# Performance work log

Hardware: AMD Instinct MI355X
Metric: run time of the kernel (lower is better)

The kernel has to match this reference:

```python
import jax, jax.numpy as jnp
import numpy as np

B, T, D = 4, 2048, 1024
H = 16
HD = D // H

def setup_inputs() -> dict:
    key = jax.random.key(0)
    ks = jax.random.split(key, 3)
    x = jax.random.normal(ks[0], (B, T, D), dtype=jnp.float32)
    w_qkv = jax.random.normal(ks[1], (D, 3 * D), dtype=jnp.float32) * (1.0 / np.sqrt(D))
    b_qkv = jnp.zeros((3 * D,), dtype=jnp.float32)
    w_proj = jax.random.normal(ks[2], (D, D), dtype=jnp.float32) * (1.0 / np.sqrt(D))
    b_proj = jnp.zeros((D,), dtype=jnp.float32)
    return {"x": x, "w_qkv": w_qkv, "b_qkv": b_qkv, "w_proj": w_proj, "b_proj": b_proj}

def reference(x, w_qkv, b_qkv, w_proj, b_proj):
    b, t, c = x.shape
    qkv = x @ w_qkv + b_qkv                      # [B,T,3D]
    qkv = qkv.reshape(b, t, 3, H, HD).transpose(2, 0, 3, 1, 4)  # [3,B,H,T,HD]
    q, k, v = qkv[0], qkv[1], qkv[2]
    scale = jnp.sqrt(jnp.asarray(HD, dtype=x.dtype))
    attn = jnp.einsum('bhqd,bhkd->bhqk', q, k) / scale  # [B,H,T,T]
    causal = jnp.tril(jnp.ones((t, t), dtype=bool))
    attn = jnp.where(causal[None, None], attn, -jnp.inf)
    attn = jax.nn.softmax(attn, axis=-1)
    out = jnp.einsum('bhqk,bhkd->bhqd', attn, v)        # [B,H,T,HD]
    out = out.transpose(0, 2, 1, 3).reshape(b, t, c)
    return out @ w_proj + b_proj
```

## Files before the change

### kernel.cpp

```cpp
#include <hip/hip_runtime.h>

typedef float f32x4 __attribute__((ext_vector_type(4)));
typedef __bf16 bf16x8 __attribute__((ext_vector_type(8)));

static __device__ __forceinline__ unsigned short f2bf(float f) {
    unsigned int u = __builtin_bit_cast(unsigned int, f);
    u += 0x7fffu + ((u >> 16) & 1u);
    return (unsigned short)(u >> 16);
}
static __device__ __forceinline__ unsigned short bfc(float f) {
    return __builtin_bit_cast(unsigned short, (__bf16)f);
}

#define QSC 0.18033688011112042f

typedef const __attribute__((address_space(1))) unsigned int gu32;
typedef __attribute__((address_space(3))) unsigned int lu32;
static __device__ __forceinline__ void gload_lds16(const unsigned short* g, unsigned short* l) {
    __builtin_amdgcn_global_load_lds((gu32*)g, (lu32*)l, 16, 0, 0);
}

__global__ __launch_bounds__(256)
void cvt_bf16(const float* __restrict__ in, unsigned short* __restrict__ out) {
    int i = blockIdx.x * 256 + threadIdx.x;
    const float4* p = (const float4*)in + (size_t)i * 2;
    float4 a = p[0], b = p[1];
    union { unsigned short s[8]; uint4 v; } u;
    u.s[0] = f2bf(a.x); u.s[1] = f2bf(a.y); u.s[2] = f2bf(a.z); u.s[3] = f2bf(a.w);
    u.s[4] = f2bf(b.x); u.s[5] = f2bf(b.y); u.s[6] = f2bf(b.z); u.s[7] = f2bf(b.w);
    ((uint4*)out)[i] = u.v;
}

__global__ __launch_bounds__(256)
void transpose_w(const float* __restrict__ w, unsigned short* __restrict__ wT,
                 int K, int N) {
    __shared__ unsigned short Lt[64][65];
    const int k0 = blockIdx.x * 64, n0 = blockIdx.y * 64;
    const int t = threadIdx.x;
    const int r = t >> 4, c4 = (t & 15) * 4;
    #pragma unroll
    for (int i = 0; i < 4; i++) {
        int rr = r + i * 16;
        float4 v = *(const float4*)(w + (k0 + rr) * N + n0 + c4);
        Lt[rr][c4 + 0] = f2bf(v.x); Lt[rr][c4 + 1] = f2bf(v.y);
        Lt[rr][c4 + 2] = f2bf(v.z); Lt[rr][c4 + 3] = f2bf(v.w);
    }
    __syncthreads();
    const int rn = t >> 3, ks = (t & 7) * 8;
    #pragma unroll
    for (int i = 0; i < 2; i++) {
        int rr = rn + i * 32;
        unsigned short tmp[8];
        #pragma unroll
        for (int j = 0; j < 8; j++) tmp[j] = Lt[ks + j][rr];
        *(uint4*)(wT + (n0 + rr) * K + k0 + ks) = *(const uint4*)tmp;
    }
}

__global__ __launch_bounds__(256)
void qkv_gemm2(const unsigned short* __restrict__ A,
               const unsigned short* __restrict__ Bt,
               const float* __restrict__ bias,
               unsigned short* __restrict__ q_ws,
               unsigned short* __restrict__ k_ws,
               unsigned short* __restrict__ vT_ws)
{
    const int K = 1024;
    __shared__ unsigned short LD[16384];
    const int tid = threadIdx.x;
    const int lane = tid & 63, w = tid >> 6;
    const int l15 = lane & 15, lhi = lane >> 4;
    const int m0 = blockIdx.x * 128, n0 = blockIdx.y * 128;
    const int wm = (w >> 1) * 64, wn = (w & 1) * 64;

    const int srow = w * 32 + (lane >> 2);
    const int sg = ((lane & 3) ^ ((lane >> 3) & 3)) * 8;
    const unsigned short* ga = A + (size_t)(m0 + srow) * K + sg;
    const unsigned short* gb = Bt + (size_t)(n0 + srow) * K + sg;
    const int lofs = w * 32 * 32;

    const int rc = (lhi ^ ((l15 >> 1) & 3)) * 8;

    #define ALp(c) (LD + (c) * 4096)
    #define BLp(c) (LD + 8192 + (c) * 4096)

    f32x4 acc[4][4] = {};

    gload_lds16(ga, ALp(0) + lofs);
    gload_lds16(ga + 16 * K, ALp(0) + lofs + 512);
    gload_lds16(gb, BLp(0) + lofs);
    gload_lds16(gb + 16 * K, BLp(0) + lofs + 512);
    __syncthreads();

    int cur = 0;
    for (int k0 = 0; k0 < K; k0 += 32) {
        const int nxt = cur ^ 1;
        if (k0 + 32 < K) {
            gload_lds16(ga + k0 + 32,          ALp(nxt) + lofs);
            gload_lds16(ga + k0 + 32 + 16 * K, ALp(nxt) + lofs + 512);
            gload_lds16(gb + k0 + 32,          BLp(nxt) + lofs);
            gload_lds16(gb + k0 + 32 + 16 * K, BLp(nxt) + lofs + 512);
        }
        bf16x8 af[4], bfr[4];
        #pragma unroll
        for (int m = 0; m < 4; m++)
            af[m] = *(const bf16x8*)(ALp(cur) + (wm + m * 16 + l15) * 32 + rc);
        #pragma unroll
        for (int n = 0; n < 4; n++)
            bfr[n] = *(const bf16x8*)(BLp(cur) + (wn + n * 16 + l15) * 32 + rc);
        __builtin_amdgcn_s_setprio(1);
        #pragma unroll
        for (int m = 0; m < 4; m++)
            #pragma unroll
            for (int n = 0; n < 4; n++)
                acc[m][n] = __builtin_amdgcn_mfma_f32_16x16x32_bf16(af[m], bfr[n], acc[m][n], 0, 0, 0);
        __builtin_amdgcn_s_setprio(0);
        __syncthreads();
        cur = nxt;
    }

    const int which = n0 >> 10;
    if (which == 2) {
        #pragma unroll
        for (int n = 0; n < 4; n++) {
            int col = n0 + wn + n * 16 + l15;
            float bv = bias[col];
            int d = col & 1023;
            int h = d >> 6, hd = d & 63;
            #pragma unroll
            for (int m = 0; m < 4; m++) {
                int row0 = m0 + wm + m * 16 + lhi * 4;
                int b = row0 >> 11, t0 = row0 & 2047;
                ushort4 pk;
                pk.x = f2bf(acc[m][n][0] + bv);
                pk.y = f2bf(acc[m][n][1] + bv);
                pk.z = f2bf(acc[m][n][2] + bv);
                pk.w = f2bf(acc[m][n][3] + bv);
                *(ushort4*)(&vT_ws[((size_t)(b * 16 + h) * 64 + hd) * 2048 + t0]) = pk;
            }
        }
    } else {
        const float qs = (which == 0) ? QSC : 1.0f;
        unsigned short* q_or_k = (which == 0) ? q_ws : k_ws;
        __syncthreads();
        #pragma unroll
        for (int n = 0; n < 4; n++) {
            int col = wn + n * 16 + l15;
            float bv = bias[n0 + col];
            #pragma unroll
            for (int m = 0; m < 4; m++) {
                #pragma unroll
                for (int j = 0; j < 4; j++) {
                    int r = wm + m * 16 + lhi * 4 + j;
                    LD[r * 128 + col] = f2bf((acc[m][n][j] + bv) * qs);
                }
            }
        }
        __syncthreads();
        const int cbase = n0 & 1023;
        #pragma unroll
        for (int i = 0; i < 8; i++) {
            int e = i * 256 + tid;
            int r = e >> 4, c = (e & 15) * 8;
            uint4 v = *(const uint4*)(&LD[r * 128 + c]);
            int grow = m0 + r;
            int b = grow >> 11, t = grow & 2047;
            int gc = cbase + c;
            int h = gc >> 6, hd = gc & 63;
            *(uint4*)(&q_or_k[((size_t)(b * 16 + h) * 2048 + t) * 64 + hd]) = v;
        }
    }
    #undef ALp
    #undef BLp
}

#define LKK 72

__global__ __launch_bounds__(256, 2)
void attn_fwd(const unsigned short* __restrict__ q_ws,
              const unsigned short* __restrict__ k_ws,
              const unsigned short* __restrict__ vT_ws,
              unsigned short* __restrict__ attn_ws)
{
    __shared__ unsigned short Kb[2][64 * LKK];
    __shared__ unsigned short Vb[2][64 * LKK];
    __shared__ unsigned short Pl[4][2][16 * 64];

    const int bh = blockIdx.x;
    const int qb = 15 - blockIdx.y;
    const int b = bh >> 4, h = bh & 15;
    const int tid = threadIdx.x;
    const int lane = tid & 63, wid = tid >> 6;
    const int l15 = lane & 15, lhi = lane >> 4;
    const int tbase = bh * 2048;
    const float NINF = -__builtin_inff();

    const int r0 = tid >> 2;
    const int c0 = (tid & 3) * 16;
    const unsigned short* kg = k_ws + (size_t)(tbase + r0) * 64 + c0;
    const unsigned short* vg = vT_ws + ((size_t)bh * 64 + r0) * 2048 + c0;

    const int xr = l15 & 7;

    bf16x8 ones;
    #pragma unroll
    for (int z = 0; z < 8; z++) ones[z] = (__bf16)1.0f;

    const int qrow = qb * 128 + wid * 32;
    const int nkv = 2 * (qb + 1);

    bf16x8 qf[2][2];
    #pragma unroll
    for (int m = 0; m < 2; m++)
        #pragma unroll
        for (int ks = 0; ks < 2; ks++)
            qf[m][ks] = *(const bf16x8*)(q_ws + (size_t)(tbase + qrow + m * 16 + l15) * 64 + ks * 32 + lhi * 8);

    f32x4 o[2][4] = {};
    f32x4 osum[2] = {};

    *(uint4*)(&Kb[0][r0 * LKK + c0])     = *(const uint4*)(kg);
    *(uint4*)(&Kb[0][r0 * LKK + c0 + 8]) = *(const uint4*)(kg + 8);
    *(uint4*)(&Vb[0][r0 * LKK + c0])     = *(const uint4*)(vg);
    *(uint4*)(&Vb[0][r0 * LKK + c0 + 8]) = *(const uint4*)(vg + 8);
    __syncthreads();

    int cur = 0;
    for (int kb = 0; kb < nkv; ++kb) {
        const int k0 = kb * 64;
        const int knx = (kb + 1 < nkv ? kb + 1 : kb) * 64;
        uint4 ka0 = *(const uint4*)(kg + (size_t)knx * 64);
        uint4 ka1 = *(const uint4*)(kg + (size_t)knx * 64 + 8);
        uint4 va0 = *(const uint4*)(vg + knx);
        uint4 va1 = *(const uint4*)(vg + knx + 8);

        if (k0 <= qrow + 31) {
            f32x4 s[2][4] = {};
            __builtin_amdgcn_s_setprio(1);
            #pragma unroll
            for (int ks = 0; ks < 2; ks++) {
                bf16x8 kf[4];
                #pragma unroll
                for (int n = 0; n < 4; n++)
                    kf[n] = *(const bf16x8*)(&Kb[cur][(n * 16 + l15) * LKK + ks * 32 + lhi * 8]);
                #pragma unroll
                for (int m = 0; m < 2; m++)
                    #pragma unroll
                    for (int n = 0; n < 4; n++)
                        s[m][n] = __builtin_amdgcn_mfma_f32_16x16x32_bf16(kf[n], qf[m][ks], s[m][n], 0, 0, 0);
            }
            __builtin_amdgcn_s_setprio(0);
            if (k0 + 63 > qrow) {
                #pragma unroll
                for (int m = 0; m < 2; m++) {
                    int qg = qrow + m * 16 + l15;
                    #pragma unroll
                    for (int n = 0; n < 4; n++) {
                        int kgl = k0 + n * 16 + lhi * 4;
                        #pragma unroll
                        for (int j = 0; j < 4; j++)
                            s[m][n][j] = (kgl + j <= qg) ? s[m][n][j] : NINF;
                    }
                }
            }
            #pragma unroll
            for (int m = 0; m < 2; m++)
                #pragma unroll
                for (int n = 0; n < 4; n++)
                    #pragma unroll
                    for (int j = 0; j < 4; j++)
                        s[m][n][j] = exp2f(s[m][n][j]);
            #pragma unroll
            for (int m = 0; m < 2; m++)
                #pragma unroll
                for (int n = 0; n < 4; n++) {
                    ushort4 pk;
                    pk.x = bfc(s[m][n][0]); pk.y = bfc(s[m][n][1]);
                    pk.z = bfc(s[m][n][2]); pk.w = bfc(s[m][n][3]);
                    int chunk = (2 * n + (lhi >> 1)) ^ xr;
                    *(ushort4*)(&Pl[wid][m][l15 * 64 + chunk * 8 + (lhi & 1) * 4]) = pk;
                }
            __builtin_amdgcn_s_setprio(1);
            #pragma unroll
            for (int ks = 0; ks < 2; ks++) {
                int chunk = (4 * ks + lhi) ^ xr;
                bf16x8 vf[4];
                #pragma unroll
                for (int nd = 0; nd < 4; nd++)
                    vf[nd] = *(const bf16x8*)(&Vb[cur][(nd * 16 + l15) * LKK + ks * 32 + lhi * 8]);
                #pragma unroll
                for (int m = 0; m < 2; m++) {
                    bf16x8 pf = *(const bf16x8*)(&Pl[wid][m][l15 * 64 + chunk * 8]);
                    #pragma unroll
                    for (int nd = 0; nd < 4; nd++)
                        o[m][nd] = __builtin_amdgcn_mfma_f32_16x16x32_bf16(pf, vf[nd], o[m][nd], 0, 0, 0);
                    osum[m] = __builtin_amdgcn_mfma_f32_16x16x32_bf16(pf, ones, osum[m], 0, 0, 0);
                }
            }
            __builtin_amdgcn_s_setprio(0);
        }
        *(uint4*)(&Kb[cur ^ 1][r0 * LKK + c0])     = ka0;
        *(uint4*)(&Kb[cur ^ 1][r0 * LKK + c0 + 8]) = ka1;
        *(uint4*)(&Vb[cur ^ 1][r0 * LKK + c0])     = va0;
        *(uint4*)(&Vb[cur ^ 1][r0 * LKK + c0 + 8]) = va1;
        __syncthreads();
        cur ^= 1;
    }
    #pragma unroll
    for (int m = 0; m < 2; m++) {
        #pragma unroll
        for (int j = 0; j < 4; j++) {
            float inv = 1.0f / osum[m][j];
            int t = qrow + m * 16 + lhi * 4 + j;
            #pragma unroll
            for (int nd = 0; nd < 4; nd++) {
                int d = nd * 16 + l15;
                attn_ws[((size_t)(b * 2048 + t) * 16 + h) * 64 + d] = f2bf(o[m][nd][j] * inv);
            }
        }
    }
}

__global__ __launch_bounds__(256)
void proj_gemm2(const unsigned short* __restrict__ A,
                const unsigned short* __restrict__ Bt,
                const float* __restrict__ bias, float* __restrict__ out)
{
    const int K = 1024, N = 1024;
    __shared__ unsigned short Al[2][128 * 32];
    __shared__ unsigned short Bl[2][128 * 32];
    const int tid = threadIdx.x;
    const int lane = tid & 63, w = tid >> 6;
    const int l15 = lane & 15, lhi = lane >> 4;
    const int m0 = blockIdx.x * 128, n0 = blockIdx.y * 128;
    const int wm = (w >> 1) * 64, wn = (w & 1) * 64;

    const int srow = w * 32 + (lane >> 2);
    const int sg = ((lane & 3) ^ ((lane >> 3) & 3)) * 8;
    const unsigned short* ga = A + (size_t)(m0 + srow) * K + sg;
    const unsigned short* gb = Bt + (size_t)(n0 + srow) * K + sg;
    const int lofs = w * 32 * 32;

    const int rc = (lhi ^ ((l15 >> 1) & 3)) * 8;

    f32x4 acc[4][4] = {};

    gload_lds16(ga, &Al[0][lofs]);
    gload_lds16(ga + 16 * K, &Al[0][lofs + 512]);
    gload_lds16(gb, &Bl[0][lofs]);
    gload_lds16(gb + 16 * K, &Bl[0][lofs + 512]);
    __syncthreads();

    int cur = 0;
    for (int k0 = 0; k0 < K; k0 += 32) {
        const int nxt = cur ^ 1;
        if (k0 + 32 < K) {
            gload_lds16(ga + k0 + 32,          &Al[nxt][lofs]);
            gload_lds16(ga + k0 + 32 + 16 * K, &Al[nxt][lofs + 512]);
            gload_lds16(gb + k0 + 32,          &Bl[nxt][lofs]);
            gload_lds16(gb + k0 + 32 + 16 * K, &Bl[nxt][lofs + 512]);
        }
        bf16x8 af[4], bfr[4];
        #pragma unroll
        for (int m = 0; m < 4; m++)
            af[m] = *(const bf16x8*)(&Al[cur][(wm + m * 16 + l15) * 32 + rc]);
        #pragma unroll
        for (int n = 0; n < 4; n++)
            bfr[n] = *(const bf16x8*)(&Bl[cur][(wn + n * 16 + l15) * 32 + rc]);
        __builtin_amdgcn_s_setprio(1);
        #pragma unroll
        for (int m = 0; m < 4; m++)
            #pragma unroll
            for (int n = 0; n < 4; n++)
                acc[m][n] = __builtin_amdgcn_mfma_f32_16x16x32_bf16(af[m], bfr[n], acc[m][n], 0, 0, 0);
        __builtin_amdgcn_s_setprio(0);
        __syncthreads();
        cur = nxt;
    }

    #pragma unroll
    for (int n = 0; n < 4; n++) {
        int col = n0 + wn + n * 16 + l15;
        float bv = bias[col];
        #pragma unroll
        for (int m = 0; m < 4; m++)
            #pragma unroll
            for (int j = 0; j < 4; j++) {
                int row = m0 + wm + m * 16 + lhi * 4 + j;
                out[row * N + col] = acc[m][n][j] + bv;
            }
    }
}

extern "C" void kernel_launch(void* const* d_in, const int* in_sizes, int n_in,
                              void* d_out, int out_size, void* d_ws, size_t ws_size,
                              hipStream_t stream)
{
    const float* x      = (const float*)d_in[0];
    const float* w_qkv  = (const float*)d_in[1];
    const float* b_qkv  = (const float*)d_in[2];
    const float* w_proj = (const float*)d_in[3];
    const float* b_proj = (const float*)d_in[4];
    float* out = (float*)d_out;

    const size_t SEG = (size_t)8 * 1024 * 1024;
    unsigned short* q_ws    = (unsigned short*)d_ws;
    unsigned short* k_ws    = q_ws + SEG;
    unsigned short* vT_ws   = k_ws + SEG;
    unsigned short* attn_ws = vT_ws + SEG;

    unsigned short* x_bf   = (unsigned short*)d_out;
    unsigned short* wqkvT  = x_bf + SEG;
    unsigned short* wprojT = q_ws;

    cvt_bf16<<<4096, 256, 0, stream>>>(x, x_bf);
    transpose_w<<<dim3(16, 48), 256, 0, stream>>>(w_qkv, wqkvT, 1024, 3072);
    qkv_gemm2<<<dim3(64, 24), 256, 0, stream>>>(x_bf, wqkvT, b_qkv, q_ws, k_ws, vT_ws);
    attn_fwd<<<dim3(64, 16), 256, 0, stream>>>(q_ws, k_ws, vT_ws, attn_ws);
    transpose_w<<<dim3(16, 16), 256, 0, stream>>>(w_proj, wprojT, 1024, 1024);
    proj_gemm2<<<dim3(64, 8), 256, 0, stream>>>(attn_ws, wprojT, b_proj, out);
}
```

Baseline: 165.4 us.

## Fuse fp32-to-bf16 conversion of x into QKV GEMM A-tile loading

Result: slower. 173.0 us (+4.6%).

```diff
diff --git a/kernel.cpp b/kernel.cpp
--- a/kernel.cpp
+++ b/kernel.cpp
@@ -18,17 +18,6 @@
 typedef __attribute__((address_space(3))) unsigned int lu32;
 static __device__ __forceinline__ void gload_lds16(const unsigned short* g, unsigned short* l) {
     __builtin_amdgcn_global_load_lds((gu32*)g, (lu32*)l, 16, 0, 0);
-}
-
-__global__ __launch_bounds__(256)
-void cvt_bf16(const float* __restrict__ in, unsigned short* __restrict__ out) {
-    int i = blockIdx.x * 256 + threadIdx.x;
-    const float4* p = (const float4*)in + (size_t)i * 2;
-    float4 a = p[0], b = p[1];
-    union { unsigned short s[8]; uint4 v; } u;
-    u.s[0] = f2bf(a.x); u.s[1] = f2bf(a.y); u.s[2] = f2bf(a.z); u.s[3] = f2bf(a.w);
-    u.s[4] = f2bf(b.x); u.s[5] = f2bf(b.y); u.s[6] = f2bf(b.z); u.s[7] = f2bf(b.w);
-    ((uint4*)out)[i] = u.v;
 }
 
 __global__ __launch_bounds__(256)
@@ -58,7 +47,7 @@
 }
 
 __global__ __launch_bounds__(256)
-void qkv_gemm2(const unsigned short* __restrict__ A,
+void qkv_gemm2(const float* __restrict__ X,
                const unsigned short* __restrict__ Bt,
                const float* __restrict__ bias,
                unsigned short* __restrict__ q_ws,
@@ -75,8 +64,8 @@
 
     const int srow = w * 32 + (lane >> 2);
     const int sg = ((lane & 3) ^ ((lane >> 3) & 3)) * 8;
-    const unsigned short* ga = A + (size_t)(m0 + srow) * K + sg;
-    const unsigned short* gb = Bt + (size_t)(n0 + srow) * K + sg;
+    const float*          gaf = X  + (size_t)(m0 + srow) * K + sg;
+    const unsigned short* gb  = Bt + (size_t)(n0 + srow) * K + sg;
     const int lofs = w * 32 * 32;
 
     const int rc = (lhi ^ ((l15 >> 1) & 3)) * 8;
@@ -86,18 +75,33 @@
 
     f32x4 acc[4][4] = {};
 
-    gload_lds16(ga, ALp(0) + lofs);
-    gload_lds16(ga + 16 * K, ALp(0) + lofs + 512);
-    gload_lds16(gb, BLp(0) + lofs);
-    gload_lds16(gb + 16 * K, BLp(0) + lofs + 512);
+    {
+        float4 a0 = *(const float4*)(gaf);
+        float4 a1 = *(const float4*)(gaf + 4);
+        float4 a2 = *(const float4*)(gaf + 16 * K);
+        float4 a3 = *(const float4*)(gaf + 16 * K + 4);
+        union { unsigned short s[8]; uint4 v; } u0, u1;
+        u0.s[0]=bfc(a0.x); u0.s[1]=bfc(a0.y); u0.s[2]=bfc(a0.z); u0.s[3]=bfc(a0.w);
+        u0.s[4]=bfc(a1.x); u0.s[5]=bfc(a1.y); u0.s[6]=bfc(a1.z); u0.s[7]=bfc(a1.w);
+        u1.s[0]=bfc(a2.x); u1.s[1]=bfc(a2.y); u1.s[2]=bfc(a2.z); u1.s[3]=bfc(a2.w);
+        u1.s[4]=bfc(a3.x); u1.s[5]=bfc(a3.y); u1.s[6]=bfc(a3.z); u1.s[7]=bfc(a3.w);
+        *(uint4*)(ALp(0) + lofs + lane * 8)       = u0.v;
+        *(uint4*)(ALp(0) + lofs + 512 + lane * 8) = u1.v;
+        gload_lds16(gb, BLp(0) + lofs);
+        gload_lds16(gb + 16 * K, BLp(0) + lofs + 512);
+    }
     __syncthreads();
 
     int cur = 0;
     for (int k0 = 0; k0 < K; k0 += 32) {
         const int nxt = cur ^ 1;
-        if (k0 + 32 < K) {
-            gload_lds16(ga + k0 + 32,          ALp(nxt) + lofs);
-            gload_lds16(ga + k0 + 32 + 16 * K, ALp(nxt) + lofs + 512);
+        float4 a0, a1, a2, a3;
+        const bool more = (k0 + 32 < K);
+        if (more) {
+            a0 = *(const float4*)(gaf + k0 + 32);
+            a1 = *(const float4*)(gaf + k0 + 36);
+            a2 = *(const float4*)(gaf + k0 + 32 + 16 * K);
+            a3 = *(const float4*)(gaf + k0 + 36 + 16 * K);
             gload_lds16(gb + k0 + 32,          BLp(nxt) + lofs);
             gload_lds16(gb + k0 + 32 + 16 * K, BLp(nxt) + lofs + 512);
         }
@@ -115,6 +119,15 @@
             for (int n = 0; n < 4; n++)
                 acc[m][n] = __builtin_amdgcn_mfma_f32_16x16x32_bf16(af[m], bfr[n], acc[m][n], 0, 0, 0);
         __builtin_amdgcn_s_setprio(0);
+        if (more) {
+            union { unsigned short s[8]; uint4 v; } u0, u1;
+            u0.s[0]=bfc(a0.x); u0.s[1]=bfc(a0.y); u0.s[2]=bfc(a0.z); u0.s[3]=bfc(a0.w);
+            u0.s[4]=bfc(a1.x); u0.s[5]=bfc(a1.y); u0.s[6]=bfc(a1.z); u0.s[7]=bfc(a1.w);
+            u1.s[0]=bfc(a2.x); u1.s[1]=bfc(a2.y); u1.s[2]=bfc(a2.z); u1.s[3]=bfc(a2.w);
+            u1.s[4]=bfc(a3.x); u1.s[5]=bfc(a3.y); u1.s[6]=bfc(a3.z); u1.s[7]=bfc(a3.w);
+            *(uint4*)(ALp(nxt) + lofs + lane * 8)       = u0.v;
+            *(uint4*)(ALp(nxt) + lofs + 512 + lane * 8) = u1.v;
+        }
         __syncthreads();
         cur = nxt;
     }
@@ -409,13 +422,11 @@
     unsigned short* vT_ws   = k_ws + SEG;
     unsigned short* attn_ws = vT_ws + SEG;
 
-    unsigned short* x_bf   = (unsigned short*)d_out;
-    unsigned short* wqkvT  = x_bf + SEG;
+    unsigned short* wqkvT  = (unsigned short*)d_out;
     unsigned short* wprojT = q_ws;
 
-    cvt_bf16<<<4096, 256, 0, stream>>>(x, x_bf);
     transpose_w<<<dim3(16, 48), 256, 0, stream>>>(w_qkv, wqkvT, 1024, 3072);
-    qkv_gemm2<<<dim3(64, 24), 256, 0, stream>>>(x_bf, wqkvT, b_qkv, q_ws, k_ws, vT_ws);
+    qkv_gemm2<<<dim3(64, 24), 256, 0, stream>>>(x, wqkvT, b_qkv, q_ws, k_ws, vT_ws);
     attn_fwd<<<dim3(64, 16), 256, 0, stream>>>(q_ws, k_ws, vT_ws, attn_ws);
     transpose_w<<<dim3(16, 16), 256, 0, stream>>>(w_proj, wprojT, 1024, 1024);
     proj_gemm2<<<dim3(64, 8), 256, 0, stream>>>(attn_ws, wprojT, b_proj, out);
```
